# Kernel tuning notes

Measured on AMD Instinct MI355X. Metric: run time of the kernel, lower is better.

The kernel has to match this reference:

```python
import jax, jax.numpy as jnp
import numpy as np

FUZZY_FACTOR = 2
REG_WT = 0.0008


def setup_inputs() -> dict:
    key = jax.random.key(0)
    k1, k2 = jax.random.split(key)
    logits = jax.random.normal(k1, (2, 4, 128, 128, 128), dtype=jnp.float32)
    y_pred = jax.nn.softmax(logits, axis=1)  # module assumes softmax already applied
    image = jax.random.normal(k2, (2, 1, 128, 128, 128), dtype=jnp.float32)
    return {"y_pred": y_pred, "image": image}


def _neighbor_sum(x):
    # x: [B, K, D, H, W]; 3x3x3 ones kernel with zero center, SAME padding,
    # applied independently per (batch, cluster) channel.
    B, K, D, H, W = x.shape
    kernel = jnp.ones((1, 1, 3, 3, 3), x.dtype).at[0, 0, 1, 1, 1].set(0.0)
    y = jax.lax.conv_general_dilated(
        x.reshape(B * K, 1, D, H, W), kernel,
        window_strides=(1, 1, 1), padding="SAME",
        dimension_numbers=("NCDHW", "OIDHW", "NCDHW"))
    return y.reshape(B, K, D, H, W)


def reference(y_pred, image):
    B, K = y_pred.shape[0], y_pred.shape[1]
    N = int(np.prod(y_pred.shape[2:]))
    pred = y_pred.reshape(B, K, N)          # [B, K, N]
    img = image.reshape(B, N)               # [B, N]

    mem = pred ** FUZZY_FACTOR              # fuzzy memberships [B, K, N]

    # cluster centroids v_k = sum(img*mem)/sum(mem)  -> [B, K]
    v = jnp.sum(img[:, None, :] * mem, axis=2) / jnp.sum(mem, axis=2)

    # J_1 = sum_i mem_i * (img - v_i)^2   -> [B, N]
    J1 = jnp.sum(mem * (img[:, None, :] - v[:, :, None]) ** 2, axis=1)

    # neighbor sum of each cluster's membership map (box filter minus center)
    nb = _neighbor_sum(mem.reshape(y_pred.shape)).reshape(B, K, N)
    # sum over j != i, computed once as total - self (identical algebra)
    J_in = jnp.sum(nb, axis=1, keepdims=True) - nb  # [B, K, N]
    J2 = jnp.sum(mem * J_in, axis=1)                # [B, N]

    return jnp.mean(J1) + REG_WT * jnp.mean(J2)
```

## Files before the change

kernel.cpp:

```cpp
#include <hip/hip_runtime.h>


#define BB 2
#define KK 4
#define DD 128
#define HH 128
#define WW 128
#define PLANE (HH * WW)
#define CL (DD * PLANE)
#define SD 8
#define NBD (DD / SD)
#define HR 8
#define NBH (HH / HR)
#define NT 256

__global__ __launch_bounds__(NT) void rfcm_main(
    const float* __restrict__ yp, const float* __restrict__ img,
    double* __restrict__ ws)
{
    __shared__ double red[4 * 13];

    const int tid  = threadIdx.x;
    const int wv   = tid >> 6;
    const int L    = tid & 63;
    const int half = L >> 5;
    const int wl   = L & 31;
    const int c0   = wl << 2;

    const int bid  = blockIdx.x;
    const int xcd  = bid & 7;
    const int idx  = bid >> 3;
    const int sl   = idx >> 4;
    const int ht   = idx & 15;
    const int slab = sl * 8 + xcd;
    const int b    = slab >> 4;
    const int dsb  = slab & 15;

    const int rbase = ht * HR + (wv << 1);
    const int r     = rbase + half;
    const int d0    = dsb * SD;

    const int   gr  = half ? rbase + 2 : rbase - 1;
    const int   gH  = gr < 0 ? 0 : (gr > HH - 1 ? HH - 1 : gr);
    const float hsc = (gr >= 0 && gr <= HH - 1) ? 1.f : 0.f;

    const bool okL = (wl > 0), okR = (wl < 31);

    const float* pO = yp  + (size_t)(b * KK) * CL + (size_t)r  * WW + c0;
    const float* pH = yp  + (size_t)(b * KK) * CL + (size_t)gH * WW + c0;
    const float* pI = img + (size_t)b * CL        + (size_t)r  * WW + c0;

    float4 o0[KK], a0[KK], o1[KK], a1[KK], o2[KK], a2[KK];

    auto lplane = [&](int t, float4* o, float4* a) {
        const size_t tp = (size_t)t * PLANE;
        #pragma unroll
        for (int k = 0; k < KK; k++) {
            o[k] = *(const float4*)(pO + (size_t)k * CL + tp);
            a[k] = *(const float4*)(pH + (size_t)k * CL + tp);
        }
    };

    auto extract = [&](const float4 o4, const float4 a4, float4& m, float4& s9) {
        m.x = o4.x * o4.x; m.y = o4.y * o4.y;
        m.z = o4.z * o4.z; m.w = o4.w * o4.w;
        float4 v;
        v.x = m.x + __shfl_xor(m.x, 32, 64);
        v.y = m.y + __shfl_xor(m.y, 32, 64);
        v.z = m.z + __shfl_xor(m.z, 32, 64);
        v.w = m.w + __shfl_xor(m.w, 32, 64);
        v.x = fmaf(a4.x * a4.x, hsc, v.x);
        v.y = fmaf(a4.y * a4.y, hsc, v.y);
        v.z = fmaf(a4.z * a4.z, hsc, v.z);
        v.w = fmaf(a4.w * a4.w, hsc, v.w);
        const float vl = okL ? __shfl_up(v.w, 1, 64)   : 0.f;
        const float vr = okR ? __shfl_down(v.x, 1, 64) : 0.f;
        const float t1 = v.x + v.y, t2 = v.z + v.w;
        s9.x = vl + t1; s9.y = t1 + v.z; s9.z = v.y + t2; s9.w = t2 + vr;
    };

    lplane((d0 > 0) ? d0 - 1 : 0, o0, a0);
    lplane(d0,     o1, a1);
    lplane(d0 + 1, o2, a2);
    float4 iv = *(const float4*)(pI + (size_t)d0 * PLANE);

    float4 mp[KK], sp[KK];
    float4 Mp = make_float4(0.f,0.f,0.f,0.f), Sp = make_float4(0.f,0.f,0.f,0.f);
    #pragma unroll
    for (int k = 0; k < KK; k++) {
        extract(o0[k], a0[k], mp[k], sp[k]);
        Mp.x += mp[k].x; Mp.y += mp[k].y; Mp.z += mp[k].z; Mp.w += mp[k].w;
        Sp.x += sp[k].x; Sp.y += sp[k].y; Sp.z += sp[k].z; Sp.w += sp[k].w;
    }
    if (d0 == 0) {
        #pragma unroll
        for (int k = 0; k < KK; k++) {
            mp[k] = make_float4(0.f,0.f,0.f,0.f);
            sp[k] = make_float4(0.f,0.f,0.f,0.f);
        }
        Mp = make_float4(0.f,0.f,0.f,0.f); Sp = make_float4(0.f,0.f,0.f,0.f);
    }
    lplane(d0 + 2, o0, a0);

    float smf[KK] = {0,0,0,0}, sif[KK] = {0,0,0,0}, saf[KK] = {0,0,0,0};
    float j2f = 0.f;

    auto step = [&](int i, float4* oS, float4* aS) {
        const int t = d0 + i;
        float4 ivn = iv;
        if (i < SD - 1) ivn = *(const float4*)(pI + (size_t)(t + 1) * PLANE);
        const bool rel = (i <= SD - 3) && (t + 3 < DD);
        const size_t tp3 = (size_t)(t + 3) * PLANE;

        const float4 iv2 = make_float4(iv.x*iv.x, iv.y*iv.y, iv.z*iv.z, iv.w*iv.w);
        float4 M = make_float4(0.f,0.f,0.f,0.f), S = make_float4(0.f,0.f,0.f,0.f);
        float q = 0.f, ctt = 0.f, ctp = 0.f, cpt = 0.f;

        #pragma unroll
        for (int k = 0; k < KK; k++) {
            float4 m, s9;
            extract(oS[k], aS[k], m, s9);
            if (rel) {
                oS[k] = *(const float4*)(pO + (size_t)k * CL + tp3);
                aS[k] = *(const float4*)(pH + (size_t)k * CL + tp3);
            }
            M.x += m.x;  M.y += m.y;  M.z += m.z;  M.w += m.w;
            S.x += s9.x; S.y += s9.y; S.z += s9.z; S.w += s9.w;
            q   = fmaf(m.x,m.x,     fmaf(m.y,m.y,     fmaf(m.z,m.z,     fmaf(m.w,m.w,     q))));
            ctt = fmaf(m.x,s9.x,    fmaf(m.y,s9.y,    fmaf(m.z,s9.z,    fmaf(m.w,s9.w,    ctt))));
            ctp = fmaf(m.x,sp[k].x, fmaf(m.y,sp[k].y, fmaf(m.z,sp[k].z, fmaf(m.w,sp[k].w, ctp))));
            if (i > 0)
                cpt = fmaf(mp[k].x,s9.x, fmaf(mp[k].y,s9.y, fmaf(mp[k].z,s9.z, fmaf(mp[k].w,s9.w, cpt))));
            smf[k] += (m.x + m.y) + (m.z + m.w);
            sif[k] = fmaf(m.x,iv.x,  fmaf(m.y,iv.y,  fmaf(m.z,iv.z,  fmaf(m.w,iv.w,  sif[k]))));
            saf[k] = fmaf(m.x,iv2.x, fmaf(m.y,iv2.y, fmaf(m.z,iv2.z, fmaf(m.w,iv2.w, saf[k]))));
            mp[k] = m; sp[k] = s9;
        }

        j2f += (M.x*S.x + M.y*S.y + M.z*S.z + M.w*S.w)
             - (M.x*M.x + M.y*M.y + M.z*M.z + M.w*M.w)
             + q - ctt
             + (M.x*Sp.x + M.y*Sp.y + M.z*Sp.z + M.w*Sp.w) - ctp;
        if (i > 0)
            j2f += (Mp.x*S.x + Mp.y*S.y + Mp.z*S.z + Mp.w*S.w) - cpt;

        Mp = M; Sp = S;
        iv = ivn;
    };

    step(0, o1, a1); step(1, o2, a2); step(2, o0, a0);
    step(3, o1, a1); step(4, o2, a2); step(5, o0, a0);
    step(6, o1, a1); step(7, o2, a2);

    if (d0 + SD < DD) {
        float4 S = make_float4(0.f,0.f,0.f,0.f);
        float cpt = 0.f;
        #pragma unroll
        for (int k = 0; k < KK; k++) {
            float4 m, s9;
            extract(o0[k], a0[k], m, s9);
            S.x += s9.x; S.y += s9.y; S.z += s9.z; S.w += s9.w;
            cpt = fmaf(mp[k].x,s9.x, fmaf(mp[k].y,s9.y, fmaf(mp[k].z,s9.z, fmaf(mp[k].w,s9.w, cpt))));
        }
        j2f += (Mp.x*S.x + Mp.y*S.y + Mp.z*S.z + Mp.w*S.w) - cpt;
    }

    double qd[13];
    #pragma unroll
    for (int k = 0; k < KK; k++) {
        qd[k] = (double)smf[k]; qd[4 + k] = (double)sif[k]; qd[8 + k] = (double)saf[k];
    }
    qd[12] = (double)j2f;

    #pragma unroll
    for (int qq = 0; qq < 13; qq++) {
        double v = qd[qq];
        #pragma unroll
        for (int off = 32; off > 0; off >>= 1) v += __shfl_down(v, off, 64);
        qd[qq] = v;
    }

    const int lane = tid & 63, wid = tid >> 6;
    if (lane == 0) {
        #pragma unroll
        for (int qq = 0; qq < 13; qq++) red[wid * 13 + qq] = qd[qq];
    }
    __syncthreads();
    if (tid < 13) {
        const double sfin = red[tid] + red[13 + tid] + red[26 + tid] + red[39 + tid];
        int idxo;
        if      (tid < 4)  idxo = b * KK + tid;
        else if (tid < 8)  idxo = 8  + b * KK + (tid - 4);
        else if (tid < 12) idxo = 16 + b * KK + (tid - 8);
        else               idxo = 24;
        unsafeAtomicAdd(&ws[idxo], sfin);
    }
}

__global__ void rfcm_fin(const double* __restrict__ ws, float* __restrict__ out)
{
    if (threadIdx.x == 0 && blockIdx.x == 0) {
        double j1 = 0;
        #pragma unroll
        for (int i = 0; i < BB * KK; i++)
            j1 += ws[16 + i] - ws[8 + i] * ws[8 + i] / ws[i];
        const double invBN = 1.0 / ((double)BB * (double)DD * (double)HH * (double)WW);
        out[0] = (float)(j1 * invBN + 0.0008 * ws[24] * invBN);
    }
}

extern "C" void kernel_launch(void* const* d_in, const int* in_sizes, int n_in,
                              void* d_out, int out_size, void* d_ws, size_t ws_size,
                              hipStream_t stream) {
    const float* yp  = (const float*)d_in[0];
    const float* img = (const float*)d_in[1];
    float* out = (float*)d_out;
    double* ws = (double*)d_ws;

    hipMemsetAsync(d_ws, 0, 25 * sizeof(double), stream);

    dim3 grid(BB * NBD * NBH);
    rfcm_main<<<grid, NT, 0, stream>>>(yp, img, ws);
    rfcm_fin<<<1, 64, 0, stream>>>(ws, out);
}
```

Measured before the change: 126.8 us.

## Stage membership planes into LDS via async global_load_lds double buffering

Replaces per-thread register loads of centre and halo rows with asynchronous global-to-LDS copies of a 10-row window per cluster, double-buffered across depth planes. Vertical neighbours are now read from shared memory instead of using a cross-half shuffle plus an extra halo load. The depth slab shrinks from 8 to 4 planes, doubling the block count, and the block-to-XCD mapping changes. This cuts redundant halo traffic and raises parallelism, but adds barriers and more depth-halo reloads per slab.

```diff
diff --git a/kernel.cpp b/kernel.cpp
--- a/kernel.cpp
+++ b/kernel.cpp
@@ -7,18 +7,25 @@
 #define HH 128
 #define WW 128
 #define PLANE (HH * WW)
-#define CL (DD * PLANE)
-#define SD 8
+#define CLS ((size_t)DD * PLANE)
+#define SD 4
 #define NBD (DD / SD)
 #define HR 8
 #define NBH (HH / HR)
 #define NT 256
+#define NROW 10
+
+typedef const void __attribute__((address_space(1))) gvoid_t;
+typedef void __attribute__((address_space(3))) svoid_t;
+#define GLD(gp, lp) __builtin_amdgcn_global_load_lds((gvoid_t*)(gp), (svoid_t*)(lp), 16, 0, 0)
+#define WAIT_VM(N) __builtin_amdgcn_s_waitcnt(0x0F70 | (N))
+#define BAR() __builtin_amdgcn_s_barrier()
 
 __global__ __launch_bounds__(NT) void rfcm_main(
     const float* __restrict__ yp, const float* __restrict__ img,
     double* __restrict__ ws)
 {
-    __shared__ double red[4 * 13];
+    __shared__ __align__(16) float sbuf[2][KK][NROW][WW];
 
     const int tid  = threadIdx.x;
     const int wv   = tid >> 6;
@@ -27,68 +34,60 @@
     const int wl   = L & 31;
     const int c0   = wl << 2;
 
-    const int bid  = blockIdx.x;
-    const int xcd  = bid & 7;
-    const int idx  = bid >> 3;
-    const int sl   = idx >> 4;
-    const int ht   = idx & 15;
-    const int slab = sl * 8 + xcd;
-    const int b    = slab >> 4;
-    const int dsb  = slab & 15;
-
-    const int rbase = ht * HR + (wv << 1);
-    const int r     = rbase + half;
-    const int d0    = dsb * SD;
-
-    const int   gr  = half ? rbase + 2 : rbase - 1;
-    const int   gH  = gr < 0 ? 0 : (gr > HH - 1 ? HH - 1 : gr);
-    const float hsc = (gr >= 0 && gr <= HH - 1) ? 1.f : 0.f;
+    const int bid = blockIdx.x;
+    const int xcd = bid & 7;
+    const int j   = bid >> 3;
+    const int dsb = xcd * 4 + (j & 3);
+    const int ht  = (j >> 2) & 15;
+    const int b   = j >> 6;
+
+    const int d0 = dsb * SD;
+    const int h0 = ht * HR;
+    const int r  = h0 + (wv << 1) + half;
+
+    int rs = h0 - 1; rs = rs < 0 ? 0 : (rs > HH - 2 - NROW + 2 ? 118 : rs);
+    const float su = (r > 0)      ? 1.f : 0.f;
+    const float sd = (r < HH - 1) ? 1.f : 0.f;
+    const int sc  = r - rs;
+    const int sm1 = (r > 0      ? r - 1 : 0)      - rs;
+    const int sp1 = (r < HH - 1 ? r + 1 : HH - 1) - rs;
 
     const bool okL = (wl > 0), okR = (wl < 31);
 
-    const float* pO = yp  + (size_t)(b * KK) * CL + (size_t)r  * WW + c0;
-    const float* pH = yp  + (size_t)(b * KK) * CL + (size_t)gH * WW + c0;
-    const float* pI = img + (size_t)b * CL        + (size_t)r  * WW + c0;
-
-    float4 o0[KK], a0[KK], o1[KK], a1[KK], o2[KK], a2[KK];
-
-    auto lplane = [&](int t, float4* o, float4* a) {
-        const size_t tp = (size_t)t * PLANE;
-        #pragma unroll
-        for (int k = 0; k < KK; k++) {
-            o[k] = *(const float4*)(pO + (size_t)k * CL + tp);
-            a[k] = *(const float4*)(pH + (size_t)k * CL + tp);
-        }
+    const float* pS = yp + (size_t)(b * KK + wv) * CLS + (size_t)rs * WW + (size_t)L * 4;
+    const float* pI = img + (size_t)b * CLS + (size_t)r * WW + c0;
+
+    auto stage = [&](int t, int bi) {
+        const float* g = pS + (size_t)t * PLANE;
+        float* lb = &sbuf[bi][wv][0][0];
+        #pragma unroll
+        for (int i = 0; i < 5; i++) GLD(g + i * 256, lb + i * 256);
     };
 
-    auto extract = [&](const float4 o4, const float4 a4, float4& m, float4& s9) {
-        m.x = o4.x * o4.x; m.y = o4.y * o4.y;
-        m.z = o4.z * o4.z; m.w = o4.w * o4.w;
+    auto extract = [&](int bi, int k, float4& m, float4& s9) {
+        const float4 c  = *(const float4*)&sbuf[bi][k][sc][c0];
+        const float4 u  = *(const float4*)&sbuf[bi][k][sm1][c0];
+        const float4 dn = *(const float4*)&sbuf[bi][k][sp1][c0];
+        m.x = c.x*c.x; m.y = c.y*c.y; m.z = c.z*c.z; m.w = c.w*c.w;
         float4 v;
-        v.x = m.x + __shfl_xor(m.x, 32, 64);
-        v.y = m.y + __shfl_xor(m.y, 32, 64);
-        v.z = m.z + __shfl_xor(m.z, 32, 64);
-        v.w = m.w + __shfl_xor(m.w, 32, 64);
-        v.x = fmaf(a4.x * a4.x, hsc, v.x);
-        v.y = fmaf(a4.y * a4.y, hsc, v.y);
-        v.z = fmaf(a4.z * a4.z, hsc, v.z);
-        v.w = fmaf(a4.w * a4.w, hsc, v.w);
+        v.x = fmaf(u.x*u.x, su, fmaf(dn.x*dn.x, sd, m.x));
+        v.y = fmaf(u.y*u.y, su, fmaf(dn.y*dn.y, sd, m.y));
+        v.z = fmaf(u.z*u.z, su, fmaf(dn.z*dn.z, sd, m.z));
+        v.w = fmaf(u.w*u.w, su, fmaf(dn.w*dn.w, sd, m.w));
         const float vl = okL ? __shfl_up(v.w, 1, 64)   : 0.f;
         const float vr = okR ? __shfl_down(v.x, 1, 64) : 0.f;
         const float t1 = v.x + v.y, t2 = v.z + v.w;
         s9.x = vl + t1; s9.y = t1 + v.z; s9.z = v.y + t2; s9.w = t2 + vr;
     };
 
-    lplane((d0 > 0) ? d0 - 1 : 0, o0, a0);
-    lplane(d0,     o1, a1);
-    lplane(d0 + 1, o2, a2);
-    float4 iv = *(const float4*)(pI + (size_t)d0 * PLANE);
+    stage((d0 > 0) ? d0 - 1 : 0, 1);
+    WAIT_VM(0); BAR();
 
     float4 mp[KK], sp[KK];
     float4 Mp = make_float4(0.f,0.f,0.f,0.f), Sp = make_float4(0.f,0.f,0.f,0.f);
     #pragma unroll
     for (int k = 0; k < KK; k++) {
-        extract(o0[k], a0[k], mp[k], sp[k]);
+        extract(1, k, mp[k], sp[k]);
         Mp.x += mp[k].x; Mp.y += mp[k].y; Mp.z += mp[k].z; Mp.w += mp[k].w;
         Sp.x += sp[k].x; Sp.y += sp[k].y; Sp.z += sp[k].z; Sp.w += sp[k].w;
     }
@@ -100,65 +99,75 @@
         }
         Mp = make_float4(0.f,0.f,0.f,0.f); Sp = make_float4(0.f,0.f,0.f,0.f);
     }
-    lplane(d0 + 2, o0, a0);
+    BAR();
+
+    float4 iv = *(const float4*)(pI + (size_t)d0 * PLANE);
+    stage(d0, 0); stage(d0 + 1, 1);
+    WAIT_VM(5); BAR();
 
     float smf[KK] = {0,0,0,0}, sif[KK] = {0,0,0,0}, saf[KK] = {0,0,0,0};
     float j2f = 0.f;
 
-    auto step = [&](int i, float4* oS, float4* aS) {
-        const int t = d0 + i;
-        float4 ivn = iv;
-        if (i < SD - 1) ivn = *(const float4*)(pI + (size_t)(t + 1) * PLANE);
-        const bool rel = (i <= SD - 3) && (t + 3 < DD);
-        const size_t tp3 = (size_t)(t + 3) * PLANE;
-
+    auto cstep = [&](int bi, bool g) {
         const float4 iv2 = make_float4(iv.x*iv.x, iv.y*iv.y, iv.z*iv.z, iv.w*iv.w);
         float4 M = make_float4(0.f,0.f,0.f,0.f), S = make_float4(0.f,0.f,0.f,0.f);
         float q = 0.f, ctt = 0.f, ctp = 0.f, cpt = 0.f;
-
         #pragma unroll
         for (int k = 0; k < KK; k++) {
             float4 m, s9;
-            extract(oS[k], aS[k], m, s9);
-            if (rel) {
-                oS[k] = *(const float4*)(pO + (size_t)k * CL + tp3);
-                aS[k] = *(const float4*)(pH + (size_t)k * CL + tp3);
-            }
+            extract(bi, k, m, s9);
             M.x += m.x;  M.y += m.y;  M.z += m.z;  M.w += m.w;
             S.x += s9.x; S.y += s9.y; S.z += s9.z; S.w += s9.w;
             q   = fmaf(m.x,m.x,     fmaf(m.y,m.y,     fmaf(m.z,m.z,     fmaf(m.w,m.w,     q))));
             ctt = fmaf(m.x,s9.x,    fmaf(m.y,s9.y,    fmaf(m.z,s9.z,    fmaf(m.w,s9.w,    ctt))));
             ctp = fmaf(m.x,sp[k].x, fmaf(m.y,sp[k].y, fmaf(m.z,sp[k].z, fmaf(m.w,sp[k].w, ctp))));
-            if (i > 0)
+            if (g)
                 cpt = fmaf(mp[k].x,s9.x, fmaf(mp[k].y,s9.y, fmaf(mp[k].z,s9.z, fmaf(mp[k].w,s9.w, cpt))));
             smf[k] += (m.x + m.y) + (m.z + m.w);
             sif[k] = fmaf(m.x,iv.x,  fmaf(m.y,iv.y,  fmaf(m.z,iv.z,  fmaf(m.w,iv.w,  sif[k]))));
             saf[k] = fmaf(m.x,iv2.x, fmaf(m.y,iv2.y, fmaf(m.z,iv2.z, fmaf(m.w,iv2.w, saf[k]))));
             mp[k] = m; sp[k] = s9;
         }
-
         j2f += (M.x*S.x + M.y*S.y + M.z*S.z + M.w*S.w)
              - (M.x*M.x + M.y*M.y + M.z*M.z + M.w*M.w)
              + q - ctt
              + (M.x*Sp.x + M.y*Sp.y + M.z*Sp.z + M.w*Sp.w) - ctp;
-        if (i > 0)
+        if (g)
             j2f += (Mp.x*S.x + Mp.y*S.y + Mp.z*S.z + Mp.w*S.w) - cpt;
-
         Mp = M; Sp = S;
-        iv = ivn;
     };
 
-    step(0, o1, a1); step(1, o2, a2); step(2, o0, a0);
-    step(3, o1, a1); step(4, o2, a2); step(5, o0, a0);
-    step(6, o1, a1); step(7, o2, a2);
-
-    if (d0 + SD < DD) {
+    const bool E = (d0 + SD < DD);
+    float4 ivn;
+
+    cstep(0, false);
+    BAR();
+    ivn = *(const float4*)(pI + (size_t)(d0 + 1) * PLANE);
+    stage(d0 + 2, 0);
+    WAIT_VM(5); BAR(); iv = ivn;
+
+    cstep(1, true);
+    BAR();
+    ivn = *(const float4*)(pI + (size_t)(d0 + 2) * PLANE);
+    stage(d0 + 3, 1);
+    WAIT_VM(5); BAR(); iv = ivn;
+
+    cstep(0, true);
+    BAR();
+    ivn = *(const float4*)(pI + (size_t)(d0 + 3) * PLANE);
+    if (E) { stage(d0 + 4, 0); WAIT_VM(5); } else { WAIT_VM(0); }
+    BAR(); iv = ivn;
+
+    cstep(1, true);
+
+    if (E) {
+        WAIT_VM(0); BAR();
         float4 S = make_float4(0.f,0.f,0.f,0.f);
         float cpt = 0.f;
         #pragma unroll
         for (int k = 0; k < KK; k++) {
             float4 m, s9;
-            extract(o0[k], a0[k], m, s9);
+            extract(0, k, m, s9);
             S.x += s9.x; S.y += s9.y; S.z += s9.z; S.w += s9.w;
             cpt = fmaf(mp[k].x,s9.x, fmaf(mp[k].y,s9.y, fmaf(mp[k].z,s9.z, fmaf(mp[k].w,s9.w, cpt))));
         }
@@ -180,10 +189,11 @@
         qd[qq] = v;
     }
 
-    const int lane = tid & 63, wid = tid >> 6;
-    if (lane == 0) {
-        #pragma unroll
-        for (int qq = 0; qq < 13; qq++) red[wid * 13 + qq] = qd[qq];
+    __syncthreads();
+    double* red = (double*)&sbuf[0][0][0][0];
+    if (L == 0) {
+        #pragma unroll
+        for (int qq = 0; qq < 13; qq++) red[wv * 13 + qq] = qd[qq];
     }
     __syncthreads();
     if (tid < 13) {
```

Measured after the change: 144.0 us. +13.6%, slower.
